# Kernel tuning notes

Hardware: AMD Instinct MI355X
Metric: run time of the kernel (lower is better)

The kernel has to match this reference:

```python
import jax, jax.numpy as jnp
import numpy as np

B, T, N_EMBD = 1, 512, 768
N_HEAD, N_KV_HEAD = 12, 6
HEAD_DIM = N_EMBD // N_HEAD  # 64


def rms_norm(x, eps=1e-6):
    return x * jax.lax.rsqrt(jnp.mean(x * x, axis=-1, keepdims=True) + eps)


def apply_rotary_emb(x, cos, sin):
    # x: [B, T, H, D]; cos/sin: [T, D//2]
    d2 = x.shape[-1] // 2
    x1, x2 = x[..., :d2], x[..., d2:]
    c = cos[None, :, None, :]
    s = sin[None, :, None, :]
    return jnp.concatenate([x1 * c - x2 * s, x2 * c + x1 * s], axis=-1)


def tropical_dot_product(q, k):
    # q: [B,H,T,D], k: [B,H,S,D] -> max-plus score [B,H,T,S]
    return jnp.max(q[..., :, None, :] + k[..., None, :, :], axis=-1)


def setup_inputs() -> dict:
    key = jax.random.key(0)
    ks = jax.random.split(key, 5)
    x = jax.random.normal(ks[0], (B, T, N_EMBD), dtype=jnp.float32)
    # Real RoPE tables
    half = HEAD_DIM // 2
    inv_freq = 1.0 / (10000.0 ** (np.arange(0, half, dtype=np.float32) / half))
    t = np.arange(T, dtype=np.float32)
    freqs = np.outer(t, inv_freq)  # [T, D//2]
    cos = jnp.asarray(np.cos(freqs), dtype=jnp.float32)
    sin = jnp.asarray(np.sin(freqs), dtype=jnp.float32)
    std = 0.02
    Wq = std * jax.random.normal(ks[1], (N_EMBD, N_HEAD * HEAD_DIM), dtype=jnp.float32)
    Wk = std * jax.random.normal(ks[2], (N_EMBD, N_KV_HEAD * HEAD_DIM), dtype=jnp.float32)
    Wv = std * jax.random.normal(ks[3], (N_EMBD, N_KV_HEAD * HEAD_DIM), dtype=jnp.float32)
    Wproj = std * jax.random.normal(ks[4], (N_EMBD, N_EMBD), dtype=jnp.float32)
    return {"x": x, "cos": cos, "sin": sin, "Wq": Wq, "Wk": Wk, "Wv": Wv, "Wproj": Wproj}


def reference(x, cos, sin, Wq, Wk, Wv, Wproj):
    b, t, c = x.shape
    q = (x @ Wq).reshape(b, t, N_HEAD, HEAD_DIM)
    k = (x @ Wk).reshape(b, t, N_KV_HEAD, HEAD_DIM)
    v = (x @ Wv).reshape(b, t, N_KV_HEAD, HEAD_DIM)
    q = rms_norm(apply_rotary_emb(q, cos, sin))
    k = rms_norm(apply_rotary_emb(k, cos, sin))
    q = jnp.transpose(q, (0, 2, 1, 3))  # [B,H,T,D]
    k = jnp.transpose(k, (0, 2, 1, 3))  # [B,Hkv,T,D]
    v = jnp.transpose(v, (0, 2, 1, 3))
    n_rep = N_HEAD // N_KV_HEAD
    if n_rep > 1:
        k = jnp.repeat(k, n_rep, axis=1)
        v = jnp.repeat(v, n_rep, axis=1)
    scores = tropical_dot_product(q, k)  # [B,H,T,T]
    causal = jnp.tril(jnp.ones((t, t), dtype=jnp.bool_))
    scores = scores + jnp.where(causal, 0.0, -jnp.inf)
    attn = jax.nn.softmax(scores, axis=-1)
    y = jnp.einsum('bhqk,bhkd->bhqd', attn, v)
    y = jnp.transpose(y, (0, 2, 1, 3)).reshape(b, t, c)
    return y @ Wproj
```

## Files before the change

kernel.cpp:

```cpp
#include <hip/hip_runtime.h>
#include <hip/hip_bf16.h>
#include <math.h>

#define TT   512
#define CEMB 768
#define NH   12
#define NKV  6
#define HD   64
#define KVC  (NKV*HD)

typedef short short8 __attribute__((ext_vector_type(8)));
typedef float floatx4 __attribute__((ext_vector_type(4)));

__device__ __forceinline__ unsigned pack_bf16(float lo, float hi){
  __hip_bfloat162 h = __float22bfloat162_rn(make_float2(lo, hi));
  return *reinterpret_cast<unsigned*>(&h);
}
__device__ __forceinline__ unsigned short bf16_rn(float f){
  unsigned u = __float_as_uint(f);
  u += 0x7FFFu + ((u>>16)&1u);
  return (unsigned short)(u>>16);
}

__global__ void __launch_bounds__(256) gemm_qkv_mfma(
    const float* __restrict__ X,
    const float* __restrict__ Wq, const float* __restrict__ Wk, const float* __restrict__ Wv,
    const float* __restrict__ Wp,
    const float* __restrict__ cosb, const float* __restrict__ sinb,
    float* __restrict__ q, float* __restrict__ k, float* __restrict__ v,
    unsigned short* __restrict__ WpF){
  int bx = blockIdx.x;
  if (bx >= 192){
    int t0 = (bx-192)*256 + threadIdx.x;
    for(int g=0; g<8; ++g){
      int u  = g*9216 + t0;
      int kp = u / 192;
      int n4 = (u - kp*192)*4;
      int kk = kp*2;
      float4 w0 = *(const float4*)&Wp[(size_t)kk*CEMB + n4];
      float4 w1 = *(const float4*)&Wp[(size_t)(kk+1)*CEMB + n4];
      int ks = kk>>5, qq = (kk>>3)&3, j = kk&7;
      #pragma unroll
      for(int i=0;i<4;i++){
        int n = n4+i, ct = n>>4, r = n&15;
        *(unsigned*)&WpF[ (((size_t)(ct*24 + ks)*64 + qq*16 + r)<<3) + j ] =
          pack_bf16((&w0.x)[i], (&w1.x)[i]);
      }
    }
    return;
  }
  int mt = bx / 24, nt = bx % 24;
  const float* W; int ldb, bcol;
  if (nt < 12)      { W = Wq; ldb = CEMB; bcol = nt*64; }
  else if (nt < 18) { W = Wk; ldb = KVC;  bcol = (nt-12)*64; }
  else              { W = Wv; ldb = KVC;  bcol = (nt-18)*64; }

  __shared__ __align__(16) unsigned short Al[2][64][40];
  __shared__ __align__(16) unsigned short Bl[2][64][40];

  int tid = threadIdx.x;
  int am  = tid>>2,  akg = (tid&3)*8;
  int bkp = tid>>4,  bn4 = (tid&15)*4;
  int w = tid>>6, lane = tid&63, qq = lane>>4, r = lane&15;

  floatx4 acc[4];
  #pragma unroll
  for(int c=0;c<4;c++) acc[c] = (floatx4){0.f,0.f,0.f,0.f};

  const float* Ap = X + (size_t)(mt*64 + am)*CEMB + akg;
  const float* Bp = W + (size_t)(2*bkp)*ldb + bcol + bn4;

  float4 a0 = *(const float4*)(Ap);
  float4 a1 = *(const float4*)(Ap + 4);
  float4 b0 = *(const float4*)(Bp);
  float4 b1 = *(const float4*)(Bp + ldb);

  int buf = 0;
  for(int k0=0; k0<CEMB; k0+=32){
    unsigned p0 = pack_bf16(a0.x,a0.y), p1 = pack_bf16(a0.z,a0.w);
    unsigned p2 = pack_bf16(a1.x,a1.y), p3 = pack_bf16(a1.z,a1.w);
    *(uint4*)&Al[buf][am][akg] = make_uint4(p0,p1,p2,p3);
    #pragma unroll
    for(int i=0;i<4;i++)
      *(unsigned*)&Bl[buf][bn4+i][2*bkp] = pack_bf16((&b0.x)[i], (&b1.x)[i]);
    if (k0 + 32 < CEMB){
      a0 = *(const float4*)(Ap + k0+32);
      a1 = *(const float4*)(Ap + k0+36);
      b0 = *(const float4*)(Bp + (size_t)(k0+32)*ldb);
      b1 = *(const float4*)(Bp + (size_t)(k0+33)*ldb);
    }
    __syncthreads();
    short8 af = *(short8*)&Al[buf][w*16 + r][qq*8];
    #pragma unroll
    for(int c=0;c<4;c++){
      short8 bf = *(short8*)&Bl[buf][c*16 + r][qq*8];
      acc[c] = __builtin_amdgcn_mfma_f32_16x16x32_bf16(af, bf, acc[c], 0,0,0);
    }
    buf ^= 1;
  }

  #pragma unroll
  for(int reg=0; reg<4; ++reg){
    int t = mt*64 + w*16 + qq*4 + reg;
    if (nt < 18){
      float cs0 = cosb[t*32 + r],      sn0 = sinb[t*32 + r];
      float cs1 = cosb[t*32 + 16 + r], sn1 = sinb[t*32 + 16 + r];
      float x0 = acc[0][reg], x1 = acc[1][reg], x2 = acc[2][reg], x3 = acc[3][reg];
      float n0 = x0*cs0 - x2*sn0;
      float n1 = x1*cs1 - x3*sn1;
      float n2 = x2*cs0 + x0*sn0;
      float n3 = x3*cs1 + x1*sn1;
      float ss = n0*n0 + n1*n1 + n2*n2 + n3*n3;
      ss += __shfl_xor(ss,1); ss += __shfl_xor(ss,2);
      ss += __shfl_xor(ss,4); ss += __shfl_xor(ss,8);
      float sc = rsqrtf(ss*(1.0f/64.0f) + 1e-6f);
      float* dst = (nt < 12) ? (q + (size_t)t*CEMB + nt*64)
                             : (k + (size_t)t*KVC + (nt-12)*64);
      dst[r]    = n0*sc; dst[16+r] = n1*sc;
      dst[32+r] = n2*sc; dst[48+r] = n3*sc;
    } else {
      float* dst = v + (size_t)t*KVC + (nt-18)*64;
      dst[r]    = acc[0][reg]; dst[16+r] = acc[1][reg];
      dst[32+r] = acc[2][reg]; dst[48+r] = acc[3][reg];
    }
  }
}

__global__ void __launch_bounds__(256) attn_tile(const float* __restrict__ qn,
    const float* __restrict__ kn, const float* __restrict__ vr,
    float* __restrict__ part_acc, float2* __restrict__ part_ml){
  __shared__ float QPsh[64*68];
  __shared__ float Ksh[64*64];
  __shared__ float Vsh[64*64];

  int h   = blockIdx.y;
  int idx = blockIdx.x;
  int qt = 0, rem = idx;
  while (rem > qt){ rem -= (qt+1); ++qt; }
  int ct = rem;
  int t0 = ct*64;

  int kvh  = h >> 1;
  int w    = threadIdx.x >> 6;
  int lane = threadIdx.x & 63;
  int lg   = lane >> 4;
  int lc   = lane & 15;

  #pragma unroll
  for(int sub=0; sub<4; ++sub){
    int rr = w*16 + sub*4 + lg;
    int sw = ((lc ^ (rr>>2)) & 15)*4;
    *(float4*)&QPsh[rr*68 + lc*4] =
      *(const float4*)&qn[(size_t)(qt*64+rr)*CEMB + h*HD + lc*4];
    *(float4*)&Ksh[rr*64 + sw] =
      *(const float4*)&kn[(size_t)(t0+rr)*KVC + kvh*HD + lc*4];
    *(float4*)&Vsh[rr*64 + sw] =
      *(const float4*)&vr[(size_t)(t0+rr)*KVC + kvh*HD + lc*4];
  }
  __syncthreads();

  float s[4][4];
  #pragma unroll
  for(int r=0;r<4;r++)
    #pragma unroll
    for(int c=0;c<4;c++) s[r][c] = -INFINITY;

  #pragma unroll
  for(int dg=0; dg<16; ++dg){
    float4 k4[4], q4[4];
    int ksw = ((dg ^ lc)&15)*4;
    #pragma unroll
    for(int c=0;c<4;c++)
      k4[c] = *(const float4*)&Ksh[(lc*4+c)*64 + ksw];
    #pragma unroll
    for(int r=0;r<4;r++)
      q4[r] = *(const float4*)&QPsh[(w*16+lg*4+r)*68 + dg*4];
    #pragma unroll
    for(int r=0;r<4;r++)
      #pragma unroll
      for(int c=0;c<4;c++)
        s[r][c] = fmaxf(s[r][c],
                  fmaxf(fmaxf(q4[r].x + k4[c].x, q4[r].y + k4[c].y),
                        fmaxf(q4[r].z + k4[c].z, q4[r].w + k4[c].w)));
  }

  float mrow[4], lrow[4];
  #pragma unroll
  for(int r=0;r<4;r++){
    int i = qt*64 + w*16 + lg*4 + r;
    #pragma unroll
    for(int c=0;c<4;c++)
      if (t0 + lc*4 + c > i) s[r][c] = -INFINITY;
    float mt = fmaxf(fmaxf(s[r][0],s[r][1]), fmaxf(s[r][2],s[r][3]));
    mt = fmaxf(mt, __shfl_xor(mt,1));
    mt = fmaxf(mt, __shfl_xor(mt,2));
    mt = fmaxf(mt, __shfl_xor(mt,4));
    mt = fmaxf(mt, __shfl_xor(mt,8));
    float p0 = __expf(s[r][0]-mt), p1 = __expf(s[r][1]-mt);
    float p2 = __expf(s[r][2]-mt), p3 = __expf(s[r][3]-mt);
    float ps = p0+p1+p2+p3;
    ps += __shfl_xor(ps,1); ps += __shfl_xor(ps,2);
    ps += __shfl_xor(ps,4); ps += __shfl_xor(ps,8);
    mrow[r] = mt; lrow[r] = ps;
    *(float4*)&QPsh[(w*16+lg*4+r)*68 + lc*4] = make_float4(p0,p1,p2,p3);
  }
  __builtin_amdgcn_wave_barrier();

  float acc[4][4];
  #pragma unroll
  for(int r=0;r<4;r++)
    #pragma unroll
    for(int c=0;c<4;c++) acc[r][c] = 0.f;

  #pragma unroll
  for(int jg=0; jg<16; ++jg){
    float4 v4[4], p4[4];
    int vsw = ((lc ^ jg)&15)*4;
    #pragma unroll
    for(int jj=0;jj<4;jj++)
      v4[jj] = *(const float4*)&Vsh[(jg*4+jj)*64 + vsw];
    #pragma unroll
    for(int r=0;r<4;r++)
      p4[r] = *(const float4*)&QPsh[(w*16+lg*4+r)*68 + jg*4];
    #pragma unroll
    for(int r=0;r<4;r++)
      #pragma unroll
      for(int c=0;c<4;c++)
        acc[r][c] = fmaf(p4[r].x, (&v4[0].x)[c], fmaf(p4[r].y, (&v4[1].x)[c],
                    fmaf(p4[r].z, (&v4[2].x)[c], fmaf(p4[r].w, (&v4[3].x)[c], acc[r][c]))));
  }

  #pragma unroll
  for(int r=0;r<4;r++){
    int i = qt*64 + w*16 + lg*4 + r;
    int pidx = (h*TT + i)*8 + ct;
    *(float4*)&part_acc[(size_t)pidx*64 + lc*4] =
      make_float4(acc[r][0],acc[r][1],acc[r][2],acc[r][3]);
    if (lc == 0) part_ml[pidx] = make_float2(mrow[r], lrow[r]);
  }
}

__global__ void __launch_bounds__(256) attn_reduce(const float* __restrict__ part_acc,
    const float2* __restrict__ part_ml, unsigned short* __restrict__ yF){
  int wid  = (blockIdx.x * blockDim.x + threadIdx.x) >> 6;
  int lane = threadIdx.x & 63;
  int h = wid >> 9;
  int i = wid & 511;
  int nch = (i >> 6) + 1;
  float m = -INFINITY, l = 0.f, a = 0.f;
  for(int c=0;c<nch;c++){
    int pidx = (h*TT + i)*8 + c;
    float2 ml = part_ml[pidx];
    float ac  = part_acc[(size_t)pidx*64 + lane];
    float m_new = fmaxf(m, ml.x);
    float sa  = __expf(m - m_new);
    float sc_ = __expf(ml.x - m_new);
    l = l*sa + ml.y*sc_;
    a = a*sa + ac*sc_;
    m = m_new;
  }
  float val = a / l;
  int s = i>>4, rr = i&15;
  int ks = h*2 + (lane>>5), q2 = (lane>>3)&3, j = lane&7;
  yF[ (((size_t)(s*24 + ks)*64 + q2*16 + rr)<<3) + j ] = bf16_rn(val);
}

__global__ void __launch_bounds__(256) gemm_proj_mfma(
    const unsigned short* __restrict__ yF, const unsigned short* __restrict__ WpF,
    float* __restrict__ out){
  int bx = blockIdx.x;
  int mt = bx / 12, nt = bx % 12;
  int tid = threadIdx.x, w = tid>>6, lane = tid&63, qq = lane>>4, r = lane&15;
  int s = mt*4 + w;

  const short8* Af = (const short8*)yF  + (size_t)s*24*64 + lane;
  const short8* Bf = (const short8*)WpF + lane;

  floatx4 acc[4];
  #pragma unroll
  for(int c=0;c<4;c++) acc[c] = (floatx4){0.f,0.f,0.f,0.f};

  short8 ac_ = Af[0];
  short8 bc_[4];
  #pragma unroll
  for(int c=0;c<4;c++) bc_[c] = Bf[(size_t)((nt*4+c)*24)*64];

  for(int ks=0; ks<24; ++ks){
    short8 an; short8 bn[4];
    if (ks < 23){
      an = Af[(size_t)(ks+1)*64];
      #pragma unroll
      for(int c=0;c<4;c++) bn[c] = Bf[(size_t)((nt*4+c)*24 + ks+1)*64];
    }
    #pragma unroll
    for(int c=0;c<4;c++)
      acc[c] = __builtin_amdgcn_mfma_f32_16x16x32_bf16(ac_, bc_[c], acc[c], 0,0,0);
    if (ks < 23){
      ac_ = an;
      #pragma unroll
      for(int c=0;c<4;c++) bc_[c] = bn[c];
    }
  }

  #pragma unroll
  for(int reg=0; reg<4; ++reg){
    int t = mt*64 + w*16 + qq*4 + reg;
    float* dst = out + (size_t)t*CEMB + nt*64;
    #pragma unroll
    for(int c=0;c<4;c++)
      dst[c*16 + r] = acc[c][reg];
  }
}

extern "C" void kernel_launch(void* const* d_in, const int* in_sizes, int n_in,
                              void* d_out, int out_size, void* d_ws, size_t ws_size,
                              hipStream_t stream){
  const float* x    = (const float*)d_in[0];
  const float* cosb = (const float*)d_in[1];
  const float* sinb = (const float*)d_in[2];
  const float* Wq   = (const float*)d_in[3];
  const float* Wk   = (const float*)d_in[4];
  const float* Wv   = (const float*)d_in[5];
  const float* Wp   = (const float*)d_in[6];
  float* out = (float*)d_out;

  float* ws        = (float*)d_ws;
  float* q_raw     = ws;
  float* k_raw     = q_raw + (size_t)TT*CEMB;
  float* v_raw     = k_raw + (size_t)TT*KVC;
  float* part_acc  = v_raw + (size_t)TT*KVC;
  float2* part_ml  = (float2*)(part_acc + (size_t)NH*TT*8*64);
  unsigned short* WpF = (unsigned short*)(part_ml + (size_t)NH*TT*8);
  unsigned short* yF  = WpF + (size_t)48*24*64*8;

  gemm_qkv_mfma <<<dim3(228),   256, 0, stream>>>(x, Wq, Wk, Wv, Wp, cosb, sinb,
                                                  q_raw, k_raw, v_raw, WpF);
  attn_tile     <<<dim3(36,NH), 256, 0, stream>>>(q_raw, k_raw, v_raw, part_acc, part_ml);
  attn_reduce   <<<dim3(NH*TT/4), 256, 0, stream>>>(part_acc, part_ml, yF);
  gemm_proj_mfma<<<dim3(96),    256, 0, stream>>>(yF, WpF, out);
}
```

Measured before the change: 120.9 us.

## Fuse attention split-reduce into projection GEMM with per-row-tile blocks

Merges the attn_reduce kernel into the output projection. Each of 8 blocks of 1024 threads first combines the partial softmax results for its 64 rows across all heads, writes the bf16 rows to global memory, synchronises, and then computes all 12 output column tiles for those rows. This removes one kernel launch and the gap between the two kernels. The cost is that the whole stage now runs on only 8 workgroups, so the reduction and the GEMM use a small fraction of the GPU and the work is serialised within each block.

```diff
diff --git a/kernel.cpp b/kernel.cpp
--- a/kernel.cpp
+++ b/kernel.cpp
@@ -240,75 +240,83 @@
   }
 }
 
-__global__ void __launch_bounds__(256) attn_reduce(const float* __restrict__ part_acc,
-    const float2* __restrict__ part_ml, unsigned short* __restrict__ yF){
-  int wid  = (blockIdx.x * blockDim.x + threadIdx.x) >> 6;
-  int lane = threadIdx.x & 63;
-  int h = wid >> 9;
-  int i = wid & 511;
-  int nch = (i >> 6) + 1;
-  float m = -INFINITY, l = 0.f, a = 0.f;
-  for(int c=0;c<nch;c++){
-    int pidx = (h*TT + i)*8 + c;
-    float2 ml = part_ml[pidx];
-    float ac  = part_acc[(size_t)pidx*64 + lane];
-    float m_new = fmaxf(m, ml.x);
-    float sa  = __expf(m - m_new);
-    float sc_ = __expf(ml.x - m_new);
-    l = l*sa + ml.y*sc_;
-    a = a*sa + ac*sc_;
-    m = m_new;
-  }
-  float val = a / l;
-  int s = i>>4, rr = i&15;
-  int ks = h*2 + (lane>>5), q2 = (lane>>3)&3, j = lane&7;
-  yF[ (((size_t)(s*24 + ks)*64 + q2*16 + rr)<<3) + j ] = bf16_rn(val);
-}
-
-__global__ void __launch_bounds__(256) gemm_proj_mfma(
-    const unsigned short* __restrict__ yF, const unsigned short* __restrict__ WpF,
+__global__ void __launch_bounds__(1024) gemm_proj_fused(
+    const float* __restrict__ part_acc, const float2* __restrict__ part_ml,
+    unsigned short* __restrict__ yF, const unsigned short* __restrict__ WpF,
     float* __restrict__ out){
-  int bx = blockIdx.x;
-  int mt = bx / 12, nt = bx % 12;
-  int tid = threadIdx.x, w = tid>>6, lane = tid&63, qq = lane>>4, r = lane&15;
-  int s = mt*4 + w;
-
-  const short8* Af = (const short8*)yF  + (size_t)s*24*64 + lane;
+  int mt   = blockIdx.x;
+  int tid  = threadIdx.x;
+  int w    = tid >> 6;
+  int lane = tid & 63;
+
+  for(int pp = w; pp < 768; pp += 16){
+    int h  = pp >> 6;
+    int il = pp & 63;
+    int i  = mt*64 + il;
+    int nch = (i >> 6) + 1;
+    float m = -INFINITY, l = 0.f, a = 0.f;
+    for(int c=0;c<nch;c++){
+      int pidx = (h*TT + i)*8 + c;
+      float2 ml = part_ml[pidx];
+      float ac  = part_acc[(size_t)pidx*64 + lane];
+      float m_new = fmaxf(m, ml.x);
+      float sa  = __expf(m - m_new);
+      float sc_ = __expf(ml.x - m_new);
+      l = l*sa + ml.y*sc_;
+      a = a*sa + ac*sc_;
+      m = m_new;
+    }
+    float val = a / l;
+    int s2 = mt*4 + (il>>4), rr = il&15;
+    int ks = h*2 + (lane>>5), q2 = (lane>>3)&3, j = lane&7;
+    yF[ (((size_t)(s2*24 + ks)*64 + q2*16 + rr)<<3) + j ] = bf16_rn(val);
+  }
+  __syncthreads();
+
+  int s_local = w & 3;
+  int ng      = w >> 2;
+  int s2      = mt*4 + s_local;
+  int qq = lane>>4, r = lane&15;
+
+  const short8* Af = (const short8*)yF  + (size_t)s2*24*64 + lane;
   const short8* Bf = (const short8*)WpF + lane;
 
-  floatx4 acc[4];
-  #pragma unroll
-  for(int c=0;c<4;c++) acc[c] = (floatx4){0.f,0.f,0.f,0.f};
-
-  short8 ac_ = Af[0];
-  short8 bc_[4];
-  #pragma unroll
-  for(int c=0;c<4;c++) bc_[c] = Bf[(size_t)((nt*4+c)*24)*64];
-
-  for(int ks=0; ks<24; ++ks){
-    short8 an; short8 bn[4];
-    if (ks < 23){
-      an = Af[(size_t)(ks+1)*64];
-      #pragma unroll
-      for(int c=0;c<4;c++) bn[c] = Bf[(size_t)((nt*4+c)*24 + ks+1)*64];
-    }
-    #pragma unroll
-    for(int c=0;c<4;c++)
-      acc[c] = __builtin_amdgcn_mfma_f32_16x16x32_bf16(ac_, bc_[c], acc[c], 0,0,0);
-    if (ks < 23){
-      ac_ = an;
-      #pragma unroll
-      for(int c=0;c<4;c++) bc_[c] = bn[c];
-    }
-  }
-
-  #pragma unroll
-  for(int reg=0; reg<4; ++reg){
-    int t = mt*64 + w*16 + qq*4 + reg;
-    float* dst = out + (size_t)t*CEMB + nt*64;
-    #pragma unroll
-    for(int c=0;c<4;c++)
-      dst[c*16 + r] = acc[c][reg];
+  for(int nn=0; nn<3; ++nn){
+    int nt = ng*3 + nn;
+    floatx4 acc[4];
+    #pragma unroll
+    for(int c=0;c<4;c++) acc[c] = (floatx4){0.f,0.f,0.f,0.f};
+
+    short8 ac_ = Af[0];
+    short8 bc_[4];
+    #pragma unroll
+    for(int c=0;c<4;c++) bc_[c] = Bf[(size_t)((nt*4+c)*24)*64];
+
+    for(int ks=0; ks<24; ++ks){
+      short8 an; short8 bn[4];
+      if (ks < 23){
+        an = Af[(size_t)(ks+1)*64];
+        #pragma unroll
+        for(int c=0;c<4;c++) bn[c] = Bf[(size_t)((nt*4+c)*24 + ks+1)*64];
+      }
+      #pragma unroll
+      for(int c=0;c<4;c++)
+        acc[c] = __builtin_amdgcn_mfma_f32_16x16x32_bf16(ac_, bc_[c], acc[c], 0,0,0);
+      if (ks < 23){
+        ac_ = an;
+        #pragma unroll
+        for(int c=0;c<4;c++) bc_[c] = bn[c];
+      }
+    }
+
+    #pragma unroll
+    for(int reg=0; reg<4; ++reg){
+      int t = mt*64 + s_local*16 + qq*4 + reg;
+      float* dst = out + (size_t)t*CEMB + nt*64;
+      #pragma unroll
+      for(int c=0;c<4;c++)
+        dst[c*16 + r] = acc[c][reg];
+    }
   }
 }
 
@@ -333,9 +341,8 @@
   unsigned short* WpF = (unsigned short*)(part_ml + (size_t)NH*TT*8);
   unsigned short* yF  = WpF + (size_t)48*24*64*8;
 
-  gemm_qkv_mfma <<<dim3(228),   256, 0, stream>>>(x, Wq, Wk, Wv, Wp, cosb, sinb,
-                                                  q_raw, k_raw, v_raw, WpF);
-  attn_tile     <<<dim3(36,NH), 256, 0, stream>>>(q_raw, k_raw, v_raw, part_acc, part_ml);
-  attn_reduce   <<<dim3(NH*TT/4), 256, 0, stream>>>(part_acc, part_ml, yF);
-  gemm_proj_mfma<<<dim3(96),    256, 0, stream>>>(yF, WpF, out);
-}
+  gemm_qkv_mfma  <<<dim3(228),   256, 0, stream>>>(x, Wq, Wk, Wv, Wp, cosb, sinb,
+                                                   q_raw, k_raw, v_raw, WpF);
+  attn_tile      <<<dim3(36,NH), 256, 0, stream>>>(q_raw, k_raw, v_raw, part_acc, part_ml);
+  gemm_proj_fused<<<dim3(8),    1024, 0, stream>>>(part_acc, part_ml, yF, WpF, out);
+}
```

Result: slower. 280.3 us (+131.8%).
